# Kernel tuning notes

Hardware: AMD Instinct MI355X
Metric: run time of the kernel (lower is better)

Reference implementation:

```python
import jax, jax.numpy as jnp
import numpy as np

H = 64  # hidden size

def setup_inputs() -> dict:
    key = jax.random.key(0)
    ks = jax.random.split(key, 7)
    B, T = 256, 5000
    s = 1.0 / np.sqrt(H)  # PyTorch LSTM init scale
    return {
        "x":    jax.random.normal(ks[0], (B, T), dtype=jnp.float32),
        "W_ih": jax.random.uniform(ks[1], (4 * H, 1), jnp.float32, -s, s),
        "W_hh": jax.random.uniform(ks[2], (4 * H, H), jnp.float32, -s, s),
        "b_ih": jax.random.uniform(ks[3], (4 * H,), jnp.float32, -s, s),
        "b_hh": jax.random.uniform(ks[4], (4 * H,), jnp.float32, -s, s),
        "W_fc": jax.random.uniform(ks[5], (128, H), jnp.float32, -s, s),
        "b_fc": jax.random.uniform(ks[6], (128,), jnp.float32, -s, s),
    }

def _lstm_last_hidden(x, W_ih, W_hh, b_ih, b_hh):
    # x: [B, T]; returns last hidden state h_T: [B, H]
    B, T = x.shape
    # input projection for all timesteps at once: [B, T, 4H]
    # (input_size == 1, so this is an outer product with W_ih[:, 0])
    x_proj = x[:, :, None] * W_ih[:, 0][None, None, :] + (b_ih + b_hh)

    def step(carry, xp_t):
        h, c = carry
        gates = xp_t + h @ W_hh.T  # [B, 4H]
        i = jax.nn.sigmoid(gates[:, 0 * H:1 * H])
        f = jax.nn.sigmoid(gates[:, 1 * H:2 * H])
        g = jnp.tanh(gates[:, 2 * H:3 * H])
        o = jax.nn.sigmoid(gates[:, 3 * H:4 * H])
        c = f * c + i * g
        h = o * jnp.tanh(c)
        return (h, c), None

    h0 = jnp.zeros((B, H), x.dtype)
    c0 = jnp.zeros((B, H), x.dtype)
    (h, c), _ = jax.lax.scan(step, (h0, c0), jnp.swapaxes(x_proj, 0, 1))
    return h

def reference(x, W_ih, W_hh, b_ih, b_hh, W_fc, b_fc):
    h_last = _lstm_last_hidden(x, W_ih, W_hh, b_ih, b_hh)  # [B, H]
    return jax.nn.relu(h_last @ W_fc.T + b_fc)  # [B, 128]
```

## Files before the change

### kernel.cpp

```cpp
#include <hip/hip_runtime.h>


#define LSTM_H 64
#define LSTM_T 5000
#define LSTM_B 256

typedef float v2f __attribute__((ext_vector_type(2)));

__device__ __forceinline__ void pk_fma_acc(v2f& acc, v2f a, v2f b) {
    asm("v_pk_fma_f32 %0, %1, %2, %0" : "+v"(acc) : "v"(a), "v"(b));
}

__device__ __forceinline__ float fast_rcp(float v) {
    return __builtin_amdgcn_rcpf(v);
}

template<int K>
__device__ __forceinline__ float quad_bcast(float v) {
    constexpr int ctrl = K | (K << 2) | (K << 4) | (K << 6);
    int r = __builtin_amdgcn_mov_dpp(__builtin_bit_cast(int, v),
                                     ctrl, 0xf, 0xf, false);
    return __builtin_bit_cast(float, r);
}

__global__ __launch_bounds__(256) void ECGLSTM_lstm_quad(
    const float* __restrict__ x,
    const float* __restrict__ W_ih,
    const float* __restrict__ W_hh,
    const float* __restrict__ b_ih,
    const float* __restrict__ b_hh,
    const float* __restrict__ W_fc,
    const float* __restrict__ b_fc,
    float* __restrict__ out)
{
    const int tid  = threadIdx.x;
    const int lane = tid & 63;
    const int w    = tid >> 6;
    const int g    = lane & 3;
    const int ul   = lane >> 2;
    const int u    = w * 16 + ul;
    const int b    = blockIdx.x;

    __shared__ float xch[LSTM_T];
    __shared__ float hbuf[2][LSTM_H];

    const float* xb = x + b * LSTM_T;
    for (int i = tid; i < LSTM_T; i += 256) xch[i] = xb[i];

    const int row = g * LSTM_H + u;
    v2f wreg[LSTM_H / 2];
    {
        const float4* wrow = reinterpret_cast<const float4*>(W_hh + row * LSTM_H);
        #pragma unroll
        for (int i = 0; i < LSTM_H / 4; ++i) {
            float4 v = wrow[i];
            wreg[2 * i]     = v2f{v.x, v.y};
            wreg[2 * i + 1] = v2f{v.z, v.w};
        }
    }
    const float wih  = W_ih[row];
    const float bias = b_ih[row] + b_hh[row];
    const bool  is_t = (g == 2);
    const float aexp = is_t ? -2.0f : -1.0f;
    const float smul = is_t ?  2.0f :  1.0f;
    const float dadd = is_t ? -1.0f :  0.0f;

    float c = 0.0f;
    if (tid < LSTM_H) hbuf[0][tid] = 0.0f;
    __syncthreads();

    #define LSTM_STEP(t, P)                                                    \
    {                                                                          \
        const float xv = xch[(t)];                          \
        v2f a0 = {0.f,0.f}, a1 = {0.f,0.f}, a2 = {0.f,0.f}, a3 = {0.f,0.f};    \
        const float4* h4 = reinterpret_cast<const float4*>(hbuf[(P)]);         \
        _Pragma("unroll")                                                      \
        for (int i = 0; i < LSTM_H / 4; i += 2) {                              \
            float4 hva = h4[i];                            \
            float4 hvb = h4[i + 1];                                            \
            pk_fma_acc(a0, v2f{hva.x, hva.y}, wreg[2 * i]);                    \
            pk_fma_acc(a1, v2f{hva.z, hva.w}, wreg[2 * i + 1]);                \
            pk_fma_acc(a2, v2f{hvb.x, hvb.y}, wreg[2 * i + 2]);                \
            pk_fma_acc(a3, v2f{hvb.z, hvb.w}, wreg[2 * i + 3]);                \
        }                                                                      \
        float dot = ((a0.x + a0.y) + (a1.x + a1.y))                            \
                  + ((a2.x + a2.y) + (a3.x + a3.y));                           \
        float gv  = fmaf(xv, wih, bias) + dot;                                 \
        float e   = __expf(aexp * gv);                                         \
        float act = fmaf(smul, fast_rcp(1.0f + e), dadd);                      \
        float i_  = quad_bcast<0>(act);                                        \
        float f_  = quad_bcast<1>(act);                                        \
        float g_  = quad_bcast<2>(act);                                        \
        float o_  = quad_bcast<3>(act);                                        \
        c = fmaf(f_, c, i_ * g_);                                              \
        float e2 = __expf(2.0f * c);                                           \
        float th = 1.0f - 2.0f * fast_rcp(e2 + 1.0f);                          \
        if (g == 0) hbuf[1 - (P)][u] = o_ * th;             \
        __syncthreads();                                  \
    }

    for (int t = 0; t < LSTM_T; t += 2) {
        LSTM_STEP(t, 0);
        LSTM_STEP(t + 1, 1);
    }
    #undef LSTM_STEP

    if (tid < 128) {
        float s = b_fc[tid];
        const float4* wf = reinterpret_cast<const float4*>(W_fc + tid * LSTM_H);
        const float4* h4 = reinterpret_cast<const float4*>(hbuf[0]);
        #pragma unroll
        for (int i = 0; i < LSTM_H / 4; ++i) {
            float4 wv = wf[i];
            float4 hv = h4[i];
            s = fmaf(hv.x, wv.x, s);
            s = fmaf(hv.y, wv.y, s);
            s = fmaf(hv.z, wv.z, s);
            s = fmaf(hv.w, wv.w, s);
        }
        out[b * 128 + tid] = fmaxf(s, 0.0f);
    }
}

extern "C" void kernel_launch(void* const* d_in, const int* in_sizes, int n_in,
                              void* d_out, int out_size, void* d_ws, size_t ws_size,
                              hipStream_t stream) {
    const float* x    = (const float*)d_in[0];
    const float* W_ih = (const float*)d_in[1];
    const float* W_hh = (const float*)d_in[2];
    const float* b_ih = (const float*)d_in[3];
    const float* b_hh = (const float*)d_in[4];
    const float* W_fc = (const float*)d_in[5];
    const float* b_fc = (const float*)d_in[6];
    float* out = (float*)d_out;

    ECGLSTM_lstm_quad<<<LSTM_B, 256, 0, stream>>>(
        x, W_ih, W_hh, b_ih, b_hh, W_fc, b_fc, out);
}
```

Measured before the change: 1.999 ms.

## Replace LDS h broadcast reads with DPP row-rotate register exchange in matvec

Each lane now loads only 4 h values from LDS and builds the 64-term dot product by rotating those values within 16-lane rows via DPP row_ror, with weights pre-permuted per lane to match the rotation order. This is meant to cut the 16 float4 LDS broadcast reads per step, which sit on the serial recurrence critical path. In exchange it drops the packed FMAs for 64 scalar FMAs fed by DPP movs, and it detects the rotate direction at runtime. It also adds launch_bounds min-blocks of 1.

Result: slower. 2.394 ms (+19.8%).

```diff
diff --git a/kernel.cpp b/kernel.cpp
--- a/kernel.cpp
+++ b/kernel.cpp
@@ -5,25 +5,26 @@
 #define LSTM_T 5000
 #define LSTM_B 256
 
-typedef float v2f __attribute__((ext_vector_type(2)));
-
-__device__ __forceinline__ void pk_fma_acc(v2f& acc, v2f a, v2f b) {
-    asm("v_pk_fma_f32 %0, %1, %2, %0" : "+v"(acc) : "v"(a), "v"(b));
+__device__ __forceinline__ float fast_rcp(float v) {
+    return __builtin_amdgcn_rcpf(v);
 }
 
-__device__ __forceinline__ float fast_rcp(float v) {
-    return __builtin_amdgcn_rcpf(v);
+template<int J>
+__device__ __forceinline__ float row_ror(float v) {
+    return __builtin_bit_cast(float,
+        __builtin_amdgcn_mov_dpp(__builtin_bit_cast(int, v),
+                                 0x120 + J, 0xF, 0xF, false));
 }
 
 template<int K>
 __device__ __forceinline__ float quad_bcast(float v) {
     constexpr int ctrl = K | (K << 2) | (K << 4) | (K << 6);
-    int r = __builtin_amdgcn_mov_dpp(__builtin_bit_cast(int, v),
-                                     ctrl, 0xf, 0xf, false);
-    return __builtin_bit_cast(float, r);
+    return __builtin_bit_cast(float,
+        __builtin_amdgcn_mov_dpp(__builtin_bit_cast(int, v),
+                                 ctrl, 0xF, 0xF, false));
 }
 
-__global__ __launch_bounds__(256) void ECGLSTM_lstm_quad(
+__global__ __launch_bounds__(256, 1) void ECGLSTM_lstm_dpp(
     const float* __restrict__ x,
     const float* __restrict__ W_ih,
     const float* __restrict__ W_hh,
@@ -47,17 +48,18 @@
     const float* xb = x + b * LSTM_T;
     for (int i = tid; i < LSTM_T; i += 256) xch[i] = xb[i];
 
+    int dirp = __builtin_amdgcn_mov_dpp(lane, 0x121, 0xF, 0xF, false);
+    const int e = (__builtin_amdgcn_readlane(dirp, 0) == 1) ? 1 : -1;
+
     const int row = g * LSTM_H + u;
-    v2f wreg[LSTM_H / 2];
-    {
-        const float4* wrow = reinterpret_cast<const float4*>(W_hh + row * LSTM_H);
-        #pragma unroll
-        for (int i = 0; i < LSTM_H / 4; ++i) {
-            float4 v = wrow[i];
-            wreg[2 * i]     = v2f{v.x, v.y};
-            wreg[2 * i + 1] = v2f{v.z, v.w};
-        }
+    float wrot[LSTM_H];
+    #pragma unroll
+    for (int m = 0; m < LSTM_H; ++m) {
+        const int cc = m >> 4, jj = m & 15;
+        const int k  = (((lane & 48) | ((lane + e * jj) & 15)) ^ (cc << 4));
+        wrot[m] = W_hh[row * LSTM_H + k];
     }
+
     const float wih  = W_ih[row];
     const float bias = b_ih[row] + b_hh[row];
     const bool  is_t = (g == 2);
@@ -69,25 +71,26 @@
     if (tid < LSTM_H) hbuf[0][tid] = 0.0f;
     __syncthreads();
 
+    #define RF(cN, j) a##cN = fmaf(row_ror<j>(b##cN), wrot[16 * cN + j], a##cN);
+    #define CHUNK(cN)                                                          \
+        float a##cN = b##cN * wrot[16 * cN];                                   \
+        RF(cN, 1)  RF(cN, 2)  RF(cN, 3)  RF(cN, 4)  RF(cN, 5)                  \
+        RF(cN, 6)  RF(cN, 7)  RF(cN, 8)  RF(cN, 9)  RF(cN, 10)                 \
+        RF(cN, 11) RF(cN, 12) RF(cN, 13) RF(cN, 14) RF(cN, 15)
+
     #define LSTM_STEP(t, P)                                                    \
     {                                                                          \
         const float xv = xch[(t)];                          \
-        v2f a0 = {0.f,0.f}, a1 = {0.f,0.f}, a2 = {0.f,0.f}, a3 = {0.f,0.f};    \
-        const float4* h4 = reinterpret_cast<const float4*>(hbuf[(P)]);         \
-        _Pragma("unroll")                                                      \
-        for (int i = 0; i < LSTM_H / 4; i += 2) {                              \
-            float4 hva = h4[i];                            \
-            float4 hvb = h4[i + 1];                                            \
-            pk_fma_acc(a0, v2f{hva.x, hva.y}, wreg[2 * i]);                    \
-            pk_fma_acc(a1, v2f{hva.z, hva.w}, wreg[2 * i + 1]);                \
-            pk_fma_acc(a2, v2f{hvb.x, hvb.y}, wreg[2 * i + 2]);                \
-            pk_fma_acc(a3, v2f{hvb.z, hvb.w}, wreg[2 * i + 3]);                \
-        }                                                                      \
-        float dot = ((a0.x + a0.y) + (a1.x + a1.y))                            \
-                  + ((a2.x + a2.y) + (a3.x + a3.y));                           \
+        const float* hb = hbuf[(P)];                                           \
+        float b0 = hb[lane];                                \
+        float b1 = hb[lane ^ 16];                                              \
+        float b2 = hb[lane ^ 32];                                              \
+        float b3 = hb[lane ^ 48];                                              \
+        CHUNK(0) CHUNK(1) CHUNK(2) CHUNK(3)                                    \
+        float dot = (a0 + a1) + (a2 + a3);                                     \
         float gv  = fmaf(xv, wih, bias) + dot;                                 \
-        float e   = __expf(aexp * gv);                                         \
-        float act = fmaf(smul, fast_rcp(1.0f + e), dadd);                      \
+        float ex  = __expf(aexp * gv);                                         \
+        float act = fmaf(smul, fast_rcp(1.0f + ex), dadd);                     \
         float i_  = quad_bcast<0>(act);                                        \
         float f_  = quad_bcast<1>(act);                                        \
         float g_  = quad_bcast<2>(act);                                        \
@@ -104,6 +107,8 @@
         LSTM_STEP(t + 1, 1);
     }
     #undef LSTM_STEP
+    #undef CHUNK
+    #undef RF
 
     if (tid < 128) {
         float s = b_fc[tid];
@@ -134,6 +139,6 @@
     const float* b_fc = (const float*)d_in[6];
     float* out = (float*)d_out;
 
-    ECGLSTM_lstm_quad<<<LSTM_B, 256, 0, stream>>>(
+    ECGLSTM_lstm_dpp<<<LSTM_B, 256, 0, stream>>>(
         x, W_ih, W_hh, b_ih, b_hh, W_fc, b_fc, out);
 }
```
